# Kernel tuning notes

Measured on AMD Instinct MI355X. Metric: run time of the kernel, lower is better.

The kernel has to match this reference:

```python
import jax, jax.numpy as jnp
import numpy as np

TEMPERATURE = 0.5
NEG_FILL = -9e15


def setup_inputs() -> dict:
    key = jax.random.key(0)
    k1, k2 = jax.random.split(key)
    B, D = 8192, 128
    z_i = jax.random.normal(k1, (B, D), dtype=jnp.float32)
    z_j = jax.random.normal(k2, (B, D), dtype=jnp.float32)
    return {"z_i": z_i, "z_j": z_j}


def reference(z_i, z_j):
    B = z_i.shape[0]
    N = 2 * B
    z = jnp.concatenate([z_i, z_j], axis=0)              # [2B, D]
    sim = jnp.matmul(z, z.T) / TEMPERATURE               # [2B, 2B]
    # mask out self-similarity on the diagonal
    diag = jnp.eye(N, dtype=bool)
    sim = jnp.where(diag, NEG_FILL, sim)
    # positive pair of row k is row (k+B) mod 2B
    labels = jnp.concatenate([jnp.arange(B, N), jnp.arange(0, B)])
    # CrossEntropyLoss(reduction='sum'): sum_k logsumexp(sim[k]) - sim[k, labels[k]]
    lse = jax.nn.logsumexp(sim, axis=1)                  # [2B]
    pos = sim[jnp.arange(N), labels]                     # [2B]
    loss = jnp.sum(lse - pos)
    return loss / N
```

## Files before the change

kernel.cpp:

```cpp
#include <hip/hip_runtime.h>

#define TEMP    0.5f
#define LOG2E   1.4426950408889634f
#define C2      (LOG2E / TEMP)
#define MSHIFT  160.0f
#define LN2     0.6931471805599453f
#define NROWS   16384
#define BHALF   8192
#define DDIM    128
#define PREPB   2048

typedef __bf16 bf16x8 __attribute__((ext_vector_type(8)));
typedef float  f32x16 __attribute__((ext_vector_type(16)));

__device__ __forceinline__ float fexp2(float x) {
#if __has_builtin(__builtin_amdgcn_exp2f)
  return __builtin_amdgcn_exp2f(x);
#else
  return exp2f(x);
#endif
}

__device__ __forceinline__ unsigned short f2bf(float f) {
  unsigned int u = __float_as_uint(f);
  unsigned int r = (u + 0x7FFFu + ((u >> 16) & 1u)) >> 16;
  return (unsigned short)r;
}


__global__ void k_prep(const float* __restrict__ zi, const float* __restrict__ zj,
                       unsigned short* __restrict__ zbF,
                       float* __restrict__ S, float* __restrict__ Pp) {
  const int t   = blockIdx.x * 256 + threadIdx.x;
  const int row = t >> 5;
  const int k0  = (t & 31) * 4;
  const float* src = (row < BHALF) ? (zi + (size_t)row * DDIM)
                                   : (zj + (size_t)(row - BHALF) * DDIM);
  float4 v = *reinterpret_cast<const float4*>(src + k0);

  const int g = row >> 5, lo = row & 31, khi = k0 >> 3, j0 = k0 & 7;
  ushort4 o;
  o.x = f2bf(v.x); o.y = f2bf(v.y); o.z = f2bf(v.z); o.w = f2bf(v.w);
  *reinterpret_cast<ushort4*>(zbF + (size_t)g * 4096 + khi * 256 + lo * 8 + j0) = o;

  float dot = 0.f;
  if (row < BHALF) {
    float4 w = *reinterpret_cast<const float4*>(zj + (size_t)row * DDIM + k0);
    dot = fmaf(v.x, w.x, fmaf(v.y, w.y, fmaf(v.z, w.z, v.w * w.w)));
  }
#pragma unroll
  for (int m = 32; m >= 1; m >>= 1) dot += __shfl_xor(dot, m, 64);
  __shared__ float red[4];
  if ((threadIdx.x & 63) == 0) red[threadIdx.x >> 6] = dot;
  __syncthreads();
  if (threadIdx.x == 0) Pp[blockIdx.x] = red[0] + red[1] + red[2] + red[3];

  if (t < NROWS) S[t] = 0.f;
}

template <bool MASK>
__device__ __forceinline__ void expAcc(const f32x16& acc, float& sa, float& sb,
                                       int d, int hi) {
#pragma unroll
  for (int r = 0; r < 16; ++r) {
    float e = fexp2(fmaf(acc[r], C2, -MSHIFT));
    if (MASK) {
      const int rloc = (r & 3) + 8 * (r >> 2) + 4 * hi;
      if (rloc == d) e = 0.f;
    }
    if (r & 1) sb += e; else sa += e;
  }
}

__global__ __launch_bounds__(256, 2)
void k_main(const unsigned short* __restrict__ zbF, float* __restrict__ S) {
  const int wave = threadIdx.x >> 6;
  const int lane = threadIdx.x & 63;
  const int lo = lane & 31;
  const int hi = lane >> 5;
  const int rb = blockIdx.x & 31;
  const int cc = blockIdx.x >> 5;
  const int row0w = rb * 512 + wave * 128;

  bf16x8 b[4][8];
#pragma unroll
  for (int rt = 0; rt < 4; ++rt) {
    const unsigned short* bp = zbF + (size_t)((row0w >> 5) + rt) * 4096 + hi * 256 + lo * 8;
#pragma unroll
    for (int ks = 0; ks < 8; ++ks)
      b[rt][ks] = *reinterpret_cast<const bf16x8*>(bp + ks * 512);
  }

  const f32x16 kZ = {};
  float s[4][2];
#pragma unroll
  for (int rt = 0; rt < 4; ++rt) { s[rt][0] = 0.f; s[rt][1] = 0.f; }

  const int c0base = cc * 1024;
  const unsigned short* abase = zbF + (size_t)(c0base >> 5) * 4096 + hi * 256 + lo * 8;

  bf16x8 a[8];
#pragma unroll
  for (int ks = 0; ks < 8; ++ks)
    a[ks] = *reinterpret_cast<const bf16x8*>(abase + ks * 512);

  for (int it = 0; it < 32; ++it) {
    const int c0 = c0base + it * 32;
    const int dr = c0 - row0w;
    const bool dg = (unsigned)dr < 128u;
    const int rtd = dg ? (dr >> 5) : -1;

    f32x16 acc0 = __builtin_amdgcn_mfma_f32_32x32x16_bf16(a[0], b[0][0], kZ, 0, 0, 0);
    f32x16 acc1 = __builtin_amdgcn_mfma_f32_32x32x16_bf16(a[0], b[1][0], kZ, 0, 0, 0);
#pragma unroll
    for (int ks = 1; ks < 8; ++ks) {
      acc0 = __builtin_amdgcn_mfma_f32_32x32x16_bf16(a[ks], b[0][ks], acc0, 0, 0, 0);
      acc1 = __builtin_amdgcn_mfma_f32_32x32x16_bf16(a[ks], b[1][ks], acc1, 0, 0, 0);
    }
    if (!dg) {
      expAcc<false>(acc0, s[0][0], s[0][1], -1, hi);
      expAcc<false>(acc1, s[1][0], s[1][1], -1, hi);
    } else {
      expAcc<true>(acc0, s[0][0], s[0][1], rtd == 0 ? lo : -1, hi);
      expAcc<true>(acc1, s[1][0], s[1][1], rtd == 1 ? lo : -1, hi);
    }

    acc0 = __builtin_amdgcn_mfma_f32_32x32x16_bf16(a[0], b[2][0], kZ, 0, 0, 0);
    acc1 = __builtin_amdgcn_mfma_f32_32x32x16_bf16(a[0], b[3][0], kZ, 0, 0, 0);
#pragma unroll
    for (int ks = 1; ks < 8; ++ks) {
      acc0 = __builtin_amdgcn_mfma_f32_32x32x16_bf16(a[ks], b[2][ks], acc0, 0, 0, 0);
      acc1 = __builtin_amdgcn_mfma_f32_32x32x16_bf16(a[ks], b[3][ks], acc1, 0, 0, 0);
    }

    if (it + 1 < 32) {
      const unsigned short* ap = abase + (size_t)(it + 1) * 4096;
#pragma unroll
      for (int ks = 0; ks < 8; ++ks)
        a[ks] = *reinterpret_cast<const bf16x8*>(ap + ks * 512);
    }

    if (!dg) {
      expAcc<false>(acc0, s[2][0], s[2][1], -1, hi);
      expAcc<false>(acc1, s[3][0], s[3][1], -1, hi);
    } else {
      expAcc<true>(acc0, s[2][0], s[2][1], rtd == 2 ? lo : -1, hi);
      expAcc<true>(acc1, s[3][0], s[3][1], rtd == 3 ? lo : -1, hi);
    }
  }

#pragma unroll
  for (int rt = 0; rt < 4; ++rt) {
    float v = s[rt][0] + s[rt][1];
    v += __shfl_xor(v, 32, 64);
    if (hi == 0) atomicAdd(&S[row0w + rt * 32 + lo], v);
  }
}

__global__ void k_fin(const float* __restrict__ S, const float* __restrict__ Pp,
                      float* __restrict__ out) {
  const int t = threadIdx.x;
  float q = 0.f;
  for (int r = t; r < NROWS; r += 512)
    q += LN2 * (MSHIFT + __log2f(S[r]));
  for (int r = t; r < PREPB; r += 512)
    q -= 4.0f * Pp[r];
  __shared__ float red[512];
  red[t] = q;
  __syncthreads();
  for (int s2 = 256; s2 > 0; s2 >>= 1) {
    if (t < s2) red[t] += red[t + s2];
    __syncthreads();
  }
  if (t == 0) out[0] = red[0] / (float)NROWS;
}

extern "C" void kernel_launch(void* const* d_in, const int* in_sizes, int n_in,
                              void* d_out, int out_size, void* d_ws, size_t ws_size,
                              hipStream_t stream) {
  const float* zi = (const float*)d_in[0];
  const float* zj = (const float*)d_in[1];
  unsigned short* zbF = (unsigned short*)d_ws;
  float* S  = (float*)((char*)d_ws + (size_t)NROWS * DDIM * 2);
  float* Pp = S + NROWS;
  float* out = (float*)d_out;

  hipLaunchKernelGGL(k_prep, dim3(PREPB), dim3(256), 0, stream, zi, zj, zbF, S, Pp);
  hipLaunchKernelGGL(k_main, dim3(512),  dim3(256), 0, stream, zbF, S);
  hipLaunchKernelGGL(k_fin,  dim3(1),    dim3(512), 0, stream, S, Pp, out);
}
```

Measured before the change: 134.9 us.

## Software-pipeline MFMA tiles with exp accumulation of previous tile results

Restructures the main loop so that MFMA chains for one pair of row tiles are interleaved with exp2 accumulation of the previous pair's accumulators, keeping matrix and vector units busy together. A-fragment reloads for the next column block are also spread across the MFMA sequence. This holds two extra f32x16 accumulator pairs live, raising register pressure, which matters under launch_bounds(256,2). The final reduction kernel also moves from 512 to 1024 threads.

```diff
diff --git a/kernel.cpp b/kernel.cpp
--- a/kernel.cpp
+++ b/kernel.cpp
@@ -58,11 +58,13 @@
   if (t < NROWS) S[t] = 0.f;
 }
 
+
 template <bool MASK>
-__device__ __forceinline__ void expAcc(const f32x16& acc, float& sa, float& sb,
-                                       int d, int hi) {
-#pragma unroll
-  for (int r = 0; r < 16; ++r) {
+__device__ __forceinline__ void exp4(const f32x16& acc, int r0, float& sa, float& sb,
+                                     int d, int hi) {
+#pragma unroll
+  for (int q = 0; q < 4; ++q) {
+    const int r = r0 + q;
     float e = fexp2(fmaf(acc[r], C2, -MSHIFT));
     if (MASK) {
       const int rloc = (r & 3) + 8 * (r >> 2) + 4 * hi;
@@ -70,6 +72,40 @@
     }
     if (r & 1) sb += e; else sa += e;
   }
+}
+
+template <bool MASK, bool RELOAD>
+__device__ __forceinline__ void phase(bf16x8 (&a)[8],
+                                      const bf16x8 (&bA)[8], const bf16x8 (&bB)[8],
+                                      const unsigned short* __restrict__ ap,
+                                      f32x16& x0, f32x16& x1,
+                                      const f32x16& e0, const f32x16& e1,
+                                      float& s0a, float& s0b, float& s1a, float& s1b,
+                                      int d0, int d1, int hi) {
+  const f32x16 kZ = {};
+  x0 = __builtin_amdgcn_mfma_f32_32x32x16_bf16(a[0], bA[0], kZ, 0, 0, 0);
+  x1 = __builtin_amdgcn_mfma_f32_32x32x16_bf16(a[0], bB[0], kZ, 0, 0, 0);
+  if constexpr (RELOAD) a[0] = *reinterpret_cast<const bf16x8*>(ap);
+  exp4<MASK>(e0, 0, s0a, s0b, d0, hi);
+#pragma unroll
+  for (int ks = 1; ks < 8; ++ks) {
+    x0 = __builtin_amdgcn_mfma_f32_32x32x16_bf16(a[ks], bA[ks], x0, 0, 0, 0);
+    x1 = __builtin_amdgcn_mfma_f32_32x32x16_bf16(a[ks], bB[ks], x1, 0, 0, 0);
+    if constexpr (RELOAD)
+      a[ks] = *reinterpret_cast<const bf16x8*>(ap + (size_t)ks * 512);
+    if (ks < 4) exp4<MASK>(e0, ks * 4,       s0a, s0b, d0, hi);
+    else        exp4<MASK>(e1, (ks - 4) * 4, s1a, s1b, d1, hi);
+  }
+}
+
+template <bool MASK>
+__device__ __forceinline__ void expTail(const f32x16& e0, const f32x16& e1,
+                                        float& s0a, float& s0b, float& s1a, float& s1b,
+                                        int d0, int d1, int hi) {
+#pragma unroll
+  for (int q = 0; q < 4; ++q) exp4<MASK>(e0, q * 4, s0a, s0b, d0, hi);
+#pragma unroll
+  for (int q = 0; q < 4; ++q) exp4<MASK>(e1, q * 4, s1a, s1b, d1, hi);
 }
 
 __global__ __launch_bounds__(256, 2)
@@ -91,7 +127,6 @@
       b[rt][ks] = *reinterpret_cast<const bf16x8*>(bp + ks * 512);
   }
 
-  const f32x16 kZ = {};
   float s[4][2];
 #pragma unroll
   for (int rt = 0; rt < 4; ++rt) { s[rt][0] = 0.f; s[rt][1] = 0.f; }
@@ -103,49 +138,53 @@
 #pragma unroll
   for (int ks = 0; ks < 8; ++ks)
     a[ks] = *reinterpret_cast<const bf16x8*>(abase + ks * 512);
+
+  f32x16 accP0, accP1, accQ0, accQ1;
+
+  {
+    const f32x16 kZ = {};
+    accP0 = __builtin_amdgcn_mfma_f32_32x32x16_bf16(a[0], b[0][0], kZ, 0, 0, 0);
+    accP1 = __builtin_amdgcn_mfma_f32_32x32x16_bf16(a[0], b[1][0], kZ, 0, 0, 0);
+#pragma unroll
+    for (int ks = 1; ks < 8; ++ks) {
+      accP0 = __builtin_amdgcn_mfma_f32_32x32x16_bf16(a[ks], b[0][ks], accP0, 0, 0, 0);
+      accP1 = __builtin_amdgcn_mfma_f32_32x32x16_bf16(a[ks], b[1][ks], accP1, 0, 0, 0);
+    }
+  }
 
   for (int it = 0; it < 32; ++it) {
     const int c0 = c0base + it * 32;
     const int dr = c0 - row0w;
     const bool dg = (unsigned)dr < 128u;
     const int rtd = dg ? (dr >> 5) : -1;
-
-    f32x16 acc0 = __builtin_amdgcn_mfma_f32_32x32x16_bf16(a[0], b[0][0], kZ, 0, 0, 0);
-    f32x16 acc1 = __builtin_amdgcn_mfma_f32_32x32x16_bf16(a[0], b[1][0], kZ, 0, 0, 0);
-#pragma unroll
-    for (int ks = 1; ks < 8; ++ks) {
-      acc0 = __builtin_amdgcn_mfma_f32_32x32x16_bf16(a[ks], b[0][ks], acc0, 0, 0, 0);
-      acc1 = __builtin_amdgcn_mfma_f32_32x32x16_bf16(a[ks], b[1][ks], acc1, 0, 0, 0);
-    }
-    if (!dg) {
-      expAcc<false>(acc0, s[0][0], s[0][1], -1, hi);
-      expAcc<false>(acc1, s[1][0], s[1][1], -1, hi);
+    const unsigned short* apn = abase + (size_t)(it + 1) * 4096;
+
+    if (it < 31) {
+      if (!dg) {
+        phase<false, true >(a, b[2], b[3], apn, accQ0, accQ1, accP0, accP1,
+                            s[0][0], s[0][1], s[1][0], s[1][1], -1, -1, hi);
+        phase<false, false>(a, b[0], b[1], abase, accP0, accP1, accQ0, accQ1,
+                            s[2][0], s[2][1], s[3][0], s[3][1], -1, -1, hi);
+      } else {
+        phase<true, true >(a, b[2], b[3], apn, accQ0, accQ1, accP0, accP1,
+                           s[0][0], s[0][1], s[1][0], s[1][1],
+                           rtd == 0 ? lo : -1, rtd == 1 ? lo : -1, hi);
+        phase<true, false>(a, b[0], b[1], abase, accP0, accP1, accQ0, accQ1,
+                           s[2][0], s[2][1], s[3][0], s[3][1],
+                           rtd == 2 ? lo : -1, rtd == 3 ? lo : -1, hi);
+      }
     } else {
-      expAcc<true>(acc0, s[0][0], s[0][1], rtd == 0 ? lo : -1, hi);
-      expAcc<true>(acc1, s[1][0], s[1][1], rtd == 1 ? lo : -1, hi);
-    }
-
-    acc0 = __builtin_amdgcn_mfma_f32_32x32x16_bf16(a[0], b[2][0], kZ, 0, 0, 0);
-    acc1 = __builtin_amdgcn_mfma_f32_32x32x16_bf16(a[0], b[3][0], kZ, 0, 0, 0);
-#pragma unroll
-    for (int ks = 1; ks < 8; ++ks) {
-      acc0 = __builtin_amdgcn_mfma_f32_32x32x16_bf16(a[ks], b[2][ks], acc0, 0, 0, 0);
-      acc1 = __builtin_amdgcn_mfma_f32_32x32x16_bf16(a[ks], b[3][ks], acc1, 0, 0, 0);
-    }
-
-    if (it + 1 < 32) {
-      const unsigned short* ap = abase + (size_t)(it + 1) * 4096;
-#pragma unroll
-      for (int ks = 0; ks < 8; ++ks)
-        a[ks] = *reinterpret_cast<const bf16x8*>(ap + ks * 512);
-    }
-
-    if (!dg) {
-      expAcc<false>(acc0, s[2][0], s[2][1], -1, hi);
-      expAcc<false>(acc1, s[3][0], s[3][1], -1, hi);
-    } else {
-      expAcc<true>(acc0, s[2][0], s[2][1], rtd == 2 ? lo : -1, hi);
-      expAcc<true>(acc1, s[3][0], s[3][1], rtd == 3 ? lo : -1, hi);
+      if (!dg) {
+        phase<false, false>(a, b[2], b[3], abase, accQ0, accQ1, accP0, accP1,
+                            s[0][0], s[0][1], s[1][0], s[1][1], -1, -1, hi);
+        expTail<false>(accQ0, accQ1, s[2][0], s[2][1], s[3][0], s[3][1], -1, -1, hi);
+      } else {
+        phase<true, false>(a, b[2], b[3], abase, accQ0, accQ1, accP0, accP1,
+                           s[0][0], s[0][1], s[1][0], s[1][1],
+                           rtd == 0 ? lo : -1, rtd == 1 ? lo : -1, hi);
+        expTail<true>(accQ0, accQ1, s[2][0], s[2][1], s[3][0], s[3][1],
+                      rtd == 2 ? lo : -1, rtd == 3 ? lo : -1, hi);
+      }
     }
   }
 
@@ -161,14 +200,14 @@
                       float* __restrict__ out) {
   const int t = threadIdx.x;
   float q = 0.f;
-  for (int r = t; r < NROWS; r += 512)
+  for (int r = t; r < NROWS; r += 1024)
     q += LN2 * (MSHIFT + __log2f(S[r]));
-  for (int r = t; r < PREPB; r += 512)
+  for (int r = t; r < PREPB; r += 1024)
     q -= 4.0f * Pp[r];
-  __shared__ float red[512];
+  __shared__ float red[1024];
   red[t] = q;
   __syncthreads();
-  for (int s2 = 256; s2 > 0; s2 >>= 1) {
+  for (int s2 = 512; s2 > 0; s2 >>= 1) {
     if (t < s2) red[t] += red[t + s2];
     __syncthreads();
   }
@@ -187,5 +226,5 @@
 
   hipLaunchKernelGGL(k_prep, dim3(PREPB), dim3(256), 0, stream, zi, zj, zbF, S, Pp);
   hipLaunchKernelGGL(k_main, dim3(512),  dim3(256), 0, stream, zbF, S);
-  hipLaunchKernelGGL(k_fin,  dim3(1),    dim3(512), 0, stream, S, Pp, out);
-}
+  hipLaunchKernelGGL(k_fin,  dim3(1),    dim3(1024), 0, stream, S, Pp, out);
+}
```

Measured after the change: 211.4 us. 1.57x slower.

## Software-pipeline MFMA tiles with interleaved exp accumulation of previous tile

Applied to the files above, without the earlier changes.

Restructures the main loop so each 32x32 tile's MFMA chain is interleaved with the exp2/sum work of the previous tile, ping-ponging between two accumulators, and spreads the next A-tile reload across MFMA steps. The aim is to overlap matrix-core latency with VALU transcendental work instead of running them in separate phases. It also widens the final reduction kernel to 1024 threads. The cost is more live registers from two accumulators plus prefetched A data, which could pressure occupancy at launch_bounds(256,2).

```diff
diff --git a/kernel.cpp b/kernel.cpp
--- a/kernel.cpp
+++ b/kernel.cpp
@@ -58,18 +58,53 @@
   if (t < NROWS) S[t] = 0.f;
 }
 
+
 template <bool MASK>
-__device__ __forceinline__ void expAcc(const f32x16& acc, float& sa, float& sb,
-                                       int d, int hi) {
-#pragma unroll
-  for (int r = 0; r < 16; ++r) {
-    float e = fexp2(fmaf(acc[r], C2, -MSHIFT));
+__device__ __forceinline__ void expStep2(const f32x16& e, int ks, float& sa, float& sb,
+                                         int d, int hi) {
+  {
+    const int r = 2 * ks;
+    float v = fexp2(fmaf(e[r], C2, -MSHIFT));
     if (MASK) {
       const int rloc = (r & 3) + 8 * (r >> 2) + 4 * hi;
-      if (rloc == d) e = 0.f;
+      if (rloc == d) v = 0.f;
     }
-    if (r & 1) sb += e; else sa += e;
-  }
+    sa += v;
+  }
+  {
+    const int r = 2 * ks + 1;
+    float v = fexp2(fmaf(e[r], C2, -MSHIFT));
+    if (MASK) {
+      const int rloc = (r & 3) + 8 * (r >> 2) + 4 * hi;
+      if (rloc == d) v = 0.f;
+    }
+    sb += v;
+  }
+}
+
+template <bool MASK, bool RELOAD>
+__device__ __forceinline__ void buildExp(bf16x8 (&a)[8], const bf16x8 (&bT)[8],
+                                         const unsigned short* __restrict__ ap,
+                                         f32x16& x, const f32x16& e,
+                                         float& sa, float& sb, int d, int hi) {
+  const f32x16 kZ = {};
+  x = __builtin_amdgcn_mfma_f32_32x32x16_bf16(a[0], bT[0], kZ, 0, 0, 0);
+  if constexpr (RELOAD) a[0] = *reinterpret_cast<const bf16x8*>(ap);
+  expStep2<MASK>(e, 0, sa, sb, d, hi);
+#pragma unroll
+  for (int ks = 1; ks < 8; ++ks) {
+    x = __builtin_amdgcn_mfma_f32_32x32x16_bf16(a[ks], bT[ks], x, 0, 0, 0);
+    if constexpr (RELOAD)
+      a[ks] = *reinterpret_cast<const bf16x8*>(ap + (size_t)ks * 512);
+    expStep2<MASK>(e, ks, sa, sb, d, hi);
+  }
+}
+
+template <bool MASK>
+__device__ __forceinline__ void expFull(const f32x16& e, float& sa, float& sb,
+                                        int d, int hi) {
+#pragma unroll
+  for (int ks = 0; ks < 8; ++ks) expStep2<MASK>(e, ks, sa, sb, d, hi);
 }
 
 __global__ __launch_bounds__(256, 2)
@@ -91,7 +126,6 @@
       b[rt][ks] = *reinterpret_cast<const bf16x8*>(bp + ks * 512);
   }
 
-  const f32x16 kZ = {};
   float s[4][2];
 #pragma unroll
   for (int rt = 0; rt < 4; ++rt) { s[rt][0] = 0.f; s[rt][1] = 0.f; }
@@ -103,49 +137,44 @@
 #pragma unroll
   for (int ks = 0; ks < 8; ++ks)
     a[ks] = *reinterpret_cast<const bf16x8*>(abase + ks * 512);
+
+  f32x16 accA, accB;
+
+  {
+    const f32x16 kZ = {};
+    accA = __builtin_amdgcn_mfma_f32_32x32x16_bf16(a[0], b[0][0], kZ, 0, 0, 0);
+#pragma unroll
+    for (int ks = 1; ks < 8; ++ks)
+      accA = __builtin_amdgcn_mfma_f32_32x32x16_bf16(a[ks], b[0][ks], accA, 0, 0, 0);
+  }
 
   for (int it = 0; it < 32; ++it) {
     const int c0 = c0base + it * 32;
     const int dr = c0 - row0w;
     const bool dg = (unsigned)dr < 128u;
     const int rtd = dg ? (dr >> 5) : -1;
-
-    f32x16 acc0 = __builtin_amdgcn_mfma_f32_32x32x16_bf16(a[0], b[0][0], kZ, 0, 0, 0);
-    f32x16 acc1 = __builtin_amdgcn_mfma_f32_32x32x16_bf16(a[0], b[1][0], kZ, 0, 0, 0);
-#pragma unroll
-    for (int ks = 1; ks < 8; ++ks) {
-      acc0 = __builtin_amdgcn_mfma_f32_32x32x16_bf16(a[ks], b[0][ks], acc0, 0, 0, 0);
-      acc1 = __builtin_amdgcn_mfma_f32_32x32x16_bf16(a[ks], b[1][ks], acc1, 0, 0, 0);
-    }
+    const unsigned short* apn = abase + (size_t)(it + 1) * 4096;
+
     if (!dg) {
-      expAcc<false>(acc0, s[0][0], s[0][1], -1, hi);
-      expAcc<false>(acc1, s[1][0], s[1][1], -1, hi);
+      buildExp<false, false>(a, b[1], abase, accB, accA, s[0][0], s[0][1], -1, hi);
+      buildExp<false, false>(a, b[2], abase, accA, accB, s[1][0], s[1][1], -1, hi);
+      buildExp<false, true >(a, b[3], apn,   accB, accA, s[2][0], s[2][1], -1, hi);
+      if (it < 31)
+        buildExp<false, false>(a, b[0], abase, accA, accB, s[3][0], s[3][1], -1, hi);
+      else
+        expFull<false>(accB, s[3][0], s[3][1], -1, hi);
     } else {
-      expAcc<true>(acc0, s[0][0], s[0][1], rtd == 0 ? lo : -1, hi);
-      expAcc<true>(acc1, s[1][0], s[1][1], rtd == 1 ? lo : -1, hi);
-    }
-
-    acc0 = __builtin_amdgcn_mfma_f32_32x32x16_bf16(a[0], b[2][0], kZ, 0, 0, 0);
-    acc1 = __builtin_amdgcn_mfma_f32_32x32x16_bf16(a[0], b[3][0], kZ, 0, 0, 0);
-#pragma unroll
-    for (int ks = 1; ks < 8; ++ks) {
-      acc0 = __builtin_amdgcn_mfma_f32_32x32x16_bf16(a[ks], b[2][ks], acc0, 0, 0, 0);
-      acc1 = __builtin_amdgcn_mfma_f32_32x32x16_bf16(a[ks], b[3][ks], acc1, 0, 0, 0);
-    }
-
-    if (it + 1 < 32) {
-      const unsigned short* ap = abase + (size_t)(it + 1) * 4096;
-#pragma unroll
-      for (int ks = 0; ks < 8; ++ks)
-        a[ks] = *reinterpret_cast<const bf16x8*>(ap + ks * 512);
-    }
-
-    if (!dg) {
-      expAcc<false>(acc0, s[2][0], s[2][1], -1, hi);
-      expAcc<false>(acc1, s[3][0], s[3][1], -1, hi);
-    } else {
-      expAcc<true>(acc0, s[2][0], s[2][1], rtd == 2 ? lo : -1, hi);
-      expAcc<true>(acc1, s[3][0], s[3][1], rtd == 3 ? lo : -1, hi);
+      buildExp<true, false>(a, b[1], abase, accB, accA, s[0][0], s[0][1],
+                            rtd == 0 ? lo : -1, hi);
+      buildExp<true, false>(a, b[2], abase, accA, accB, s[1][0], s[1][1],
+                            rtd == 1 ? lo : -1, hi);
+      buildExp<true, true >(a, b[3], apn,   accB, accA, s[2][0], s[2][1],
+                            rtd == 2 ? lo : -1, hi);
+      if (it < 31)
+        buildExp<true, false>(a, b[0], abase, accA, accB, s[3][0], s[3][1],
+                              rtd == 3 ? lo : -1, hi);
+      else
+        expFull<true>(accB, s[3][0], s[3][1], rtd == 3 ? lo : -1, hi);
     }
   }
 
@@ -161,14 +190,14 @@
                       float* __restrict__ out) {
   const int t = threadIdx.x;
   float q = 0.f;
-  for (int r = t; r < NROWS; r += 512)
+  for (int r = t; r < NROWS; r += 1024)
     q += LN2 * (MSHIFT + __log2f(S[r]));
-  for (int r = t; r < PREPB; r += 512)
+  for (int r = t; r < PREPB; r += 1024)
     q -= 4.0f * Pp[r];
-  __shared__ float red[512];
+  __shared__ float red[1024];
   red[t] = q;
   __syncthreads();
-  for (int s2 = 256; s2 > 0; s2 >>= 1) {
+  for (int s2 = 512; s2 > 0; s2 >>= 1) {
     if (t < s2) red[t] += red[t + s2];
     __syncthreads();
   }
@@ -187,5 +216,5 @@
 
   hipLaunchKernelGGL(k_prep, dim3(PREPB), dim3(256), 0, stream, zi, zj, zbF, S, Pp);
   hipLaunchKernelGGL(k_main, dim3(512),  dim3(256), 0, stream, zbF, S);
-  hipLaunchKernelGGL(k_fin,  dim3(1),    dim3(512), 0, stream, S, Pp, out);
-}
+  hipLaunchKernelGGL(k_fin,  dim3(1),    dim3(1024), 0, stream, S, Pp, out);
+}
```

After: 174.2 us. +29.2%, slower.

## Use packed FMA for exp prep, stagger waves, raise MFMA priority, widen final reduce

Applied to the files above, without the earlier changes.

The exp accumulation now runs on two-wide float vectors, so the scale-and-shift can use packed FMA and the two partial sums become one vector add. Alternate waves sleep briefly before the main loop, and s_setprio raises wave priority around the MFMA chains. Together these aim to stagger waves so one wave's matrix work overlaps another's exp work. The final reduction kernel goes from 512 to 1024 threads. The priority and sleep tweaks depend on the scheduler, and the initial sleep adds a small delay.

```diff
diff --git a/kernel.cpp b/kernel.cpp
--- a/kernel.cpp
+++ b/kernel.cpp
@@ -12,6 +12,7 @@
 
 typedef __bf16 bf16x8 __attribute__((ext_vector_type(8)));
 typedef float  f32x16 __attribute__((ext_vector_type(16)));
+typedef float  f32x2  __attribute__((ext_vector_type(2)));
 
 __device__ __forceinline__ float fexp2(float x) {
 #if __has_builtin(__builtin_amdgcn_exp2f)
@@ -59,16 +60,24 @@
 }
 
 template <bool MASK>
-__device__ __forceinline__ void expAcc(const f32x16& acc, float& sa, float& sb,
-                                       int d, int hi) {
-#pragma unroll
-  for (int r = 0; r < 16; ++r) {
-    float e = fexp2(fmaf(acc[r], C2, -MSHIFT));
+__device__ __forceinline__ void expAcc(const f32x16& acc, f32x2& s, int d, int hi) {
+#pragma unroll
+  for (int k = 0; k < 8; ++k) {
+    f32x2 u;
+    u.x = acc[2 * k];
+    u.y = acc[2 * k + 1];
+    const f32x2 c2v = {C2, C2};
+    const f32x2 msv = {-MSHIFT, -MSHIFT};
+    u = __builtin_elementwise_fma(u, c2v, msv);
+    f32x2 e;
+    e.x = fexp2(u.x);
+    e.y = fexp2(u.y);
     if (MASK) {
-      const int rloc = (r & 3) + 8 * (r >> 2) + 4 * hi;
-      if (rloc == d) e = 0.f;
-    }
-    if (r & 1) sb += e; else sa += e;
+      const int r0 = 2 * k, r1 = 2 * k + 1;
+      if (((r0 & 3) + 8 * (r0 >> 2) + 4 * hi) == d) e.x = 0.f;
+      if (((r1 & 3) + 8 * (r1 >> 2) + 4 * hi) == d) e.y = 0.f;
+    }
+    s += e;
   }
 }
 
@@ -92,9 +101,9 @@
   }
 
   const f32x16 kZ = {};
-  float s[4][2];
-#pragma unroll
-  for (int rt = 0; rt < 4; ++rt) { s[rt][0] = 0.f; s[rt][1] = 0.f; }
+  f32x2 s[4];
+#pragma unroll
+  for (int rt = 0; rt < 4; ++rt) { s[rt].x = 0.f; s[rt].y = 0.f; }
 
   const int c0base = cc * 1024;
   const unsigned short* abase = zbF + (size_t)(c0base >> 5) * 4096 + hi * 256 + lo * 8;
@@ -103,6 +112,8 @@
 #pragma unroll
   for (int ks = 0; ks < 8; ++ks)
     a[ks] = *reinterpret_cast<const bf16x8*>(abase + ks * 512);
+
+  if (((blockIdx.x ^ wave) & 1) != 0) __builtin_amdgcn_s_sleep(4);
 
   for (int it = 0; it < 32; ++it) {
     const int c0 = c0base + it * 32;
@@ -110,6 +121,7 @@
     const bool dg = (unsigned)dr < 128u;
     const int rtd = dg ? (dr >> 5) : -1;
 
+    __builtin_amdgcn_s_setprio(1);
     f32x16 acc0 = __builtin_amdgcn_mfma_f32_32x32x16_bf16(a[0], b[0][0], kZ, 0, 0, 0);
     f32x16 acc1 = __builtin_amdgcn_mfma_f32_32x32x16_bf16(a[0], b[1][0], kZ, 0, 0, 0);
 #pragma unroll
@@ -117,14 +129,16 @@
       acc0 = __builtin_amdgcn_mfma_f32_32x32x16_bf16(a[ks], b[0][ks], acc0, 0, 0, 0);
       acc1 = __builtin_amdgcn_mfma_f32_32x32x16_bf16(a[ks], b[1][ks], acc1, 0, 0, 0);
     }
+    __builtin_amdgcn_s_setprio(0);
     if (!dg) {
-      expAcc<false>(acc0, s[0][0], s[0][1], -1, hi);
-      expAcc<false>(acc1, s[1][0], s[1][1], -1, hi);
+      expAcc<false>(acc0, s[0], -1, hi);
+      expAcc<false>(acc1, s[1], -1, hi);
     } else {
-      expAcc<true>(acc0, s[0][0], s[0][1], rtd == 0 ? lo : -1, hi);
-      expAcc<true>(acc1, s[1][0], s[1][1], rtd == 1 ? lo : -1, hi);
-    }
-
+      expAcc<true>(acc0, s[0], rtd == 0 ? lo : -1, hi);
+      expAcc<true>(acc1, s[1], rtd == 1 ? lo : -1, hi);
+    }
+
+    __builtin_amdgcn_s_setprio(1);
     acc0 = __builtin_amdgcn_mfma_f32_32x32x16_bf16(a[0], b[2][0], kZ, 0, 0, 0);
     acc1 = __builtin_amdgcn_mfma_f32_32x32x16_bf16(a[0], b[3][0], kZ, 0, 0, 0);
 #pragma unroll
@@ -132,6 +146,7 @@
       acc0 = __builtin_amdgcn_mfma_f32_32x32x16_bf16(a[ks], b[2][ks], acc0, 0, 0, 0);
       acc1 = __builtin_amdgcn_mfma_f32_32x32x16_bf16(a[ks], b[3][ks], acc1, 0, 0, 0);
     }
+    __builtin_amdgcn_s_setprio(0);
 
     if (it + 1 < 32) {
       const unsigned short* ap = abase + (size_t)(it + 1) * 4096;
@@ -141,17 +156,17 @@
     }
 
     if (!dg) {
-      expAcc<false>(acc0, s[2][0], s[2][1], -1, hi);
-      expAcc<false>(acc1, s[3][0], s[3][1], -1, hi);
+      expAcc<false>(acc0, s[2], -1, hi);
+      expAcc<false>(acc1, s[3], -1, hi);
     } else {
-      expAcc<true>(acc0, s[2][0], s[2][1], rtd == 2 ? lo : -1, hi);
-      expAcc<true>(acc1, s[3][0], s[3][1], rtd == 3 ? lo : -1, hi);
+      expAcc<true>(acc0, s[2], rtd == 2 ? lo : -1, hi);
+      expAcc<true>(acc1, s[3], rtd == 3 ? lo : -1, hi);
     }
   }
 
 #pragma unroll
   for (int rt = 0; rt < 4; ++rt) {
-    float v = s[rt][0] + s[rt][1];
+    float v = s[rt].x + s[rt].y;
     v += __shfl_xor(v, 32, 64);
     if (hi == 0) atomicAdd(&S[row0w + rt * 32 + lo], v);
   }
@@ -161,14 +176,14 @@
                       float* __restrict__ out) {
   const int t = threadIdx.x;
   float q = 0.f;
-  for (int r = t; r < NROWS; r += 512)
+  for (int r = t; r < NROWS; r += 1024)
     q += LN2 * (MSHIFT + __log2f(S[r]));
-  for (int r = t; r < PREPB; r += 512)
+  for (int r = t; r < PREPB; r += 1024)
     q -= 4.0f * Pp[r];
-  __shared__ float red[512];
+  __shared__ float red[1024];
   red[t] = q;
   __syncthreads();
-  for (int s2 = 256; s2 > 0; s2 >>= 1) {
+  for (int s2 = 512; s2 > 0; s2 >>= 1) {
     if (t < s2) red[t] += red[t + s2];
     __syncthreads();
   }
@@ -187,5 +202,5 @@
 
   hipLaunchKernelGGL(k_prep, dim3(PREPB), dim3(256), 0, stream, zi, zj, zbF, S, Pp);
   hipLaunchKernelGGL(k_main, dim3(512),  dim3(256), 0, stream, zbF, S);
-  hipLaunchKernelGGL(k_fin,  dim3(1),    dim3(512), 0, stream, S, Pp, out);
-}
+  hipLaunchKernelGGL(k_fin,  dim3(1),    dim3(1024), 0, stream, S, Pp, out);
+}
```

Result: faster. 130.6 us (-3.2%).
